# Performance work log

Hardware: AMD Instinct MI355X
Metric: run time of the kernel (lower is better)

## Reference

```python
import jax, jax.numpy as jnp
import numpy as np

B, N, VF, EF, DV, DE, LN = 64, 64, 32, 16, 128, 128, 4
EPS_INNER = 128.0  # BatchNorm1d(MAX_N, internal_d_vert): 2nd positional arg is eps (faithful to source bug)
EPS_BN = 1e-5


def gev_layer(v_in, e_in, evW, evb, eW, eb, vW, vb, relu=True):
    act = jax.nn.relu if relu else (lambda x: x)
    ev = v_in @ evW + evb                                   # [B,N,De]
    # outer_v_sum: ev.unsqueeze(1) + ev.unsqueeze(2) -> [B,N,N,De]
    e_out = act(e_in @ eW + eb + ev[:, None, :, :] + ev[:, :, None, :])
    per_v_e = e_out.sum(axis=1)                             # sum-aggregate over dim 1
    v_out = act(jnp.concatenate([per_v_e, v_in], axis=-1) @ vW + vb)
    return v_out, e_out


def bn_flat(v, g, b):
    # BatchNorm1d(N*VF) on [B, N*VF] in training mode (biased var)
    x = v.reshape(-1, N * VF)
    mu = x.mean(axis=0)
    var = x.var(axis=0)
    x = (x - mu) * jax.lax.rsqrt(var + EPS_BN) * g + b
    return x.reshape(-1, N, VF)


def bn_inner(v, g, b):
    # BatchNorm1d(MAX_N, eps=128) on [B, N, D]: channels are the N axis, stats over (B, D)
    mu = v.mean(axis=(0, 2), keepdims=True)
    var = v.var(axis=(0, 2), keepdims=True)
    return (v - mu) * jax.lax.rsqrt(var + EPS_INNER) * g[None, :, None] + b[None, :, None]


def setup_inputs() -> dict:
    key = jax.random.key(0)
    ks = jax.random.split(key, 24)
    s = 0.01  # force_lin_init with init_noise=0.01, biases zero
    nrm = lambda k, shp: jax.random.normal(k, shp, dtype=jnp.float32) * s
    inp = {
        "v": jax.random.normal(ks[0], (B, N, VF), dtype=jnp.float32),
        "e": jax.random.normal(ks[1], (B, N, N, EF), dtype=jnp.float32),
        "bn_in_g": jnp.ones((N * VF,), jnp.float32),
        "bn_in_b": jnp.zeros((N * VF,), jnp.float32),
        "g1_evW": nrm(ks[2], (VF, DE)), "g1_evb": jnp.zeros((DE,), jnp.float32),
        "g1_eW": nrm(ks[3], (EF, DE)), "g1_eb": jnp.zeros((DE,), jnp.float32),
        "g1_vW": nrm(ks[4], (VF + DE, DV)), "g1_vb": jnp.zeros((DV,), jnp.float32),
        "inn_evW": nrm(ks[5], (LN, DV, DE)), "inn_evb": jnp.zeros((LN, DE), jnp.float32),
        "inn_eW": nrm(ks[6], (LN, DE, DE)), "inn_eb": jnp.zeros((LN, DE), jnp.float32),
        "inn_vW": nrm(ks[7], (LN, DV + DE, DV)), "inn_vb": jnp.zeros((LN, DV), jnp.float32),
        "bn_g": jnp.ones((LN, N), jnp.float32),
        "bn_b": jnp.zeros((LN, N), jnp.float32),
        "g3_evW": nrm(ks[8], (DV, 1)), "g3_evb": jnp.zeros((1,), jnp.float32),
        "g3_eW": nrm(ks[9], (DE, 1)), "g3_eb": jnp.zeros((1,), jnp.float32),
        "g3_vW": nrm(ks[10], (DV + 1, 1)), "g3_vb": jnp.zeros((1,), jnp.float32),
    }
    return inp


def reference(v, e, bn_in_g, bn_in_b, g1_evW, g1_evb, g1_eW, g1_eb, g1_vW, g1_vb,
              inn_evW, inn_evb, inn_eW, inn_eb, inn_vW, inn_vb, bn_g, bn_b,
              g3_evW, g3_evb, g3_eW, g3_eb, g3_vW, g3_vb):
    v = bn_flat(v, bn_in_g, bn_in_b)
    v, e = gev_layer(v, e, g1_evW, g1_evb, g1_eW, g1_eb, g1_vW, g1_vb)
    for i in range(LN):
        v_next, e_next = gev_layer(v, e, inn_evW[i], inn_evb[i], inn_eW[i], inn_eb[i], inn_vW[i], inn_vb[i])
        v = v_next + v  # resnet
        e = e_next + e
        v = bn_inner(v, bn_g[i], bn_b[i])
    v, e = gev_layer(v, e, g3_evW, g3_evb, g3_eW, g3_eb, g3_vW, g3_vb, relu=False)
    return v, e
```

## Files before the change

kernel.cpp:

```cpp
#include <hip/hip_runtime.h>
#include <hip/hip_bf16.h>


typedef __bf16 bf16_t;
typedef __bf16 bf16x8 __attribute__((ext_vector_type(8)));
typedef __bf16 bf16x4 __attribute__((ext_vector_type(4)));
typedef float f32x4 __attribute__((ext_vector_type(4)));

__device__ __forceinline__ void bar_lgkm() {
  asm volatile("s_waitcnt lgkmcnt(0)\n\ts_barrier" ::: "memory");
}

__global__ __launch_bounds__(256) void k_prep(const float* __restrict__ vin,
    const float* __restrict__ g, const float* __restrict__ bt,
    const float* __restrict__ eW, float* __restrict__ v0,
    bf16_t* __restrict__ Wt, float* __restrict__ stats) {
  const int blk = blockIdx.x, tid = threadIdx.x;
  if (blk < 8) {
    int ch = blk * 256 + tid;
    float s = 0.f, s2 = 0.f;
    for (int b = 0; b < 64; ++b) { float x = vin[b * 2048 + ch]; s += x; s2 += x * x; }
    float mu = s * (1.f / 64.f);
    float var = s2 * (1.f / 64.f) - mu * mu;
    float sc = rsqrtf(var + 1e-5f) * g[ch];
    float bb = bt[ch];
    for (int b = 0; b < 64; ++b) {
      float x = vin[b * 2048 + ch];
      v0[b * 2048 + ch] = (x - mu) * sc + bb;
    }
  } else if (blk < 264) {
    int idx = (blk - 8) * 256 + tid;
    int l = idx >> 14, r = idx & 16383, n = r >> 7, k = r & 127;
    Wt[idx] = (bf16_t)eW[(l << 14) + (k << 7) + n];
  } else {
    for (int i = tid; i < 512; i += 256) stats[i] = 0.f;
  }
}

template <int K>
__global__ __launch_bounds__(256) void k_ev(const float* __restrict__ v_in,
    const float* __restrict__ W, const float* __restrict__ bias,
    float* __restrict__ out) {
  __shared__ float rows_s[8][K];
  const int r0 = blockIdx.x * 8;
  const int tid = threadIdx.x;
  const int c = tid & 127, h = tid >> 7;
  for (int idx = tid; idx < 8 * K; idx += 256) {
    int rr = idx / K, kk = idx % K;
    rows_s[rr][kk] = v_in[(r0 + rr) * K + kk];
  }
  __syncthreads();
  float acc[4];
  const float bv = bias[c];
#pragma unroll
  for (int r = 0; r < 4; ++r) acc[r] = bv;
  for (int k4 = 0; k4 < K; k4 += 4) {
    float w0 = W[(k4 + 0) * 128 + c], w1 = W[(k4 + 1) * 128 + c];
    float w2 = W[(k4 + 2) * 128 + c], w3 = W[(k4 + 3) * 128 + c];
#pragma unroll
    for (int r = 0; r < 4; ++r) {
      float4 x = *(const float4*)&rows_s[h * 4 + r][k4];
      acc[r] += x.x * w0 + x.y * w1 + x.z * w2 + x.w * w3;
    }
  }
#pragma unroll
  for (int r = 0; r < 4; ++r) out[(r0 + h * 4 + r) * 128 + c] = acc[r];
}

__global__ __launch_bounds__(256) void k_evbn(float* __restrict__ v,
    const float* __restrict__ stats, const float* __restrict__ g,
    const float* __restrict__ bt, const float* __restrict__ W,
    const float* __restrict__ bias, float* __restrict__ out) {
  __shared__ float rows_s[8][128];
  const int r0 = blockIdx.x * 8;
  const int tid = threadIdx.x;
  const int c = tid & 127, h = tid >> 7;
#pragma unroll
  for (int u = 0; u < 4; ++u) {
    int idx = u * 256 + tid;
    int rr = idx >> 7, k = idx & 127;
    int n = (r0 + rr) & 63;
    float mu = stats[n] * (1.f / 8192.f);
    float var = stats[64 + n] * (1.f / 8192.f) - mu * mu;
    float sc = rsqrtf(var + 128.f) * g[n];
    float x = (v[(r0 + rr) * 128 + k] - mu) * sc + bt[n];
    rows_s[rr][k] = x;
    v[(r0 + rr) * 128 + k] = x;
  }
  __syncthreads();
  float acc[4];
  const float bv = bias[c];
#pragma unroll
  for (int r = 0; r < 4; ++r) acc[r] = bv;
  for (int k4 = 0; k4 < 128; k4 += 4) {
    float w0 = W[(k4 + 0) * 128 + c], w1 = W[(k4 + 1) * 128 + c];
    float w2 = W[(k4 + 2) * 128 + c], w3 = W[(k4 + 3) * 128 + c];
#pragma unroll
    for (int r = 0; r < 4; ++r) {
      float4 x = *(const float4*)&rows_s[h * 4 + r][k4];
      acc[r] += x.x * w0 + x.y * w1 + x.z * w2 + x.w * w3;
    }
  }
#pragma unroll
  for (int r = 0; r < 4; ++r) out[(r0 + h * 4 + r) * 128 + c] = acc[r];
}

__global__ __launch_bounds__(256) void k_edge_g1(const float* __restrict__ e0,
    const float* __restrict__ eW, const float* __restrict__ eb,
    const float* __restrict__ ev, bf16_t* __restrict__ e_ws,
    float* __restrict__ pve) {
  __shared__ bf16_t A0s[2][64][40];
  __shared__ bf16_t Os[2][64][136];
  const int b = blockIdx.x >> 5, j0 = (blockIdx.x & 31) * 2;
  const int tid = threadIdx.x;
  const int lane = tid & 63, w = tid >> 6;
  const int quad = lane >> 4, l16 = lane & 15;
#pragma unroll
  for (int t = 0; t < 2; ++t) {
    int idx = tid + t * 256;
    int row = idx >> 3, off = (idx & 7) * 4;
    int jc = off >> 4, k = off & 15;
    f32x4 x = *(const f32x4*)&e0[((b * 64 + row) * 64 + j0) * 16 + off];
    bf16x4 y;
#pragma unroll
    for (int r = 0; r < 4; ++r) y[r] = (bf16_t)x[r];
    *(bf16x4*)&A0s[jc][row][k] = y;
    bf16x4 z = {(bf16_t)0.f, (bf16_t)0.f, (bf16_t)0.f, (bf16_t)0.f};
    *(bf16x4*)&A0s[jc][row][16 + k] = z;
  }
  const int c0[2] = {w * 32 + quad * 4, w * 32 + 16 + quad * 4};
  bf16x8 wf[2];
#pragma unroll
  for (int nt = 0; nt < 2; ++nt) {
    const int c = w * 32 + nt * 16 + l16;
#pragma unroll
    for (int jj = 0; jj < 8; ++jj)
      wf[nt][jj] = (quad < 2) ? (bf16_t)eW[(quad * 8 + jj) * 128 + c] : (bf16_t)0.f;
  }
  f32x4 acc[2][4][2];
  {
    f32x4 ebv[2], evj[2][2], evi[4][2];
#pragma unroll
    for (int nt = 0; nt < 2; ++nt) {
      ebv[nt] = *(const f32x4*)&eb[c0[nt]];
#pragma unroll
      for (int jc = 0; jc < 2; ++jc)
        evj[jc][nt] = *(const f32x4*)&ev[(b * 64 + j0 + jc) * 128 + c0[nt]];
#pragma unroll
      for (int mt = 0; mt < 4; ++mt)
        evi[mt][nt] = *(const f32x4*)&ev[(b * 64 + mt * 16 + l16) * 128 + c0[nt]];
    }
#pragma unroll
    for (int jc = 0; jc < 2; ++jc)
#pragma unroll
      for (int mt = 0; mt < 4; ++mt)
#pragma unroll
        for (int nt = 0; nt < 2; ++nt)
          acc[jc][mt][nt] = ebv[nt] + evj[jc][nt] + evi[mt][nt];
  }
  __syncthreads();
#pragma unroll
  for (int jc = 0; jc < 2; ++jc) {
#pragma unroll
    for (int mt = 0; mt < 4; ++mt) {
      bf16x8 ef = *(const bf16x8*)&A0s[jc][mt * 16 + l16][quad * 8];
#pragma unroll
      for (int nt = 0; nt < 2; ++nt)
        acc[jc][mt][nt] = __builtin_amdgcn_mfma_f32_16x16x32_bf16(wf[nt], ef, acc[jc][mt][nt], 0, 0, 0);
    }
  }
#pragma unroll
  for (int jc = 0; jc < 2; ++jc) {
#pragma unroll
    for (int nt = 0; nt < 2; ++nt) {
      f32x4 ps = {0.f, 0.f, 0.f, 0.f};
#pragma unroll
      for (int mt = 0; mt < 4; ++mt) {
        const int i = mt * 16 + l16;
        bf16x4 outv;
#pragma unroll
        for (int r = 0; r < 4; ++r) {
          float vv = fmaxf(acc[jc][mt][nt][r], 0.f);
          ps[r] += vv;
          outv[r] = (bf16_t)vv;
        }
        *(bf16x4*)&Os[jc][i][c0[nt]] = outv;
      }
#pragma unroll
      for (int m = 1; m <= 8; m <<= 1) {
#pragma unroll
        for (int r = 0; r < 4; ++r) ps[r] += __shfl_xor(ps[r], m);
      }
      if (l16 == 0) *(f32x4*)&pve[(b * 64 + j0 + jc) * 128 + c0[nt]] = ps;
    }
  }
  __syncthreads();
  {
    bf16_t* ebase = &e_ws[((size_t)(b * 64 + j0) * 64) * 128];
#pragma unroll
    for (int t = 0; t < 8; ++t) {
      int idx = tid + t * 256;
      *(int4*)&ebase[idx * 8] =
          *(const int4*)&Os[idx >> 10][(idx >> 4) & 63][(idx & 15) * 8];
    }
  }
}

__global__ __launch_bounds__(256) void k_vg1_ev(const float* __restrict__ pve,
    const float* __restrict__ v0, const float* __restrict__ vW,
    const float* __restrict__ vb, const float* __restrict__ evW,
    const float* __restrict__ evb, float* __restrict__ v, float* __restrict__ ev) {
  __shared__ float in_s[8][160];
  __shared__ float vr[8][128];
  const int r0 = blockIdx.x * 8;
  const int tid = threadIdx.x;
  const int c = tid & 127, h = tid >> 7;
#pragma unroll
  for (int u = 0; u < 4; ++u) {
    int idx = u * 256 + tid;
    int rr = idx >> 7, k = idx & 127;
    in_s[rr][k] = pve[(r0 + rr) * 128 + k];
  }
  {
    int rr = tid >> 5, k = tid & 31;
    in_s[rr][128 + k] = v0[(r0 + rr) * 32 + k];
  }
  __syncthreads();
  float acc[4];
  const float bv = vb[c];
#pragma unroll
  for (int r = 0; r < 4; ++r) acc[r] = bv;
  for (int k4 = 0; k4 < 160; k4 += 4) {
    float w0 = vW[(k4 + 0) * 128 + c], w1 = vW[(k4 + 1) * 128 + c];
    float w2 = vW[(k4 + 2) * 128 + c], w3 = vW[(k4 + 3) * 128 + c];
#pragma unroll
    for (int r = 0; r < 4; ++r) {
      float4 x = *(const float4*)&in_s[h * 4 + r][k4];
      acc[r] += x.x * w0 + x.y * w1 + x.z * w2 + x.w * w3;
    }
  }
#pragma unroll
  for (int r = 0; r < 4; ++r) {
    float val = fmaxf(acc[r], 0.f);
    vr[h * 4 + r][c] = val;
    v[(r0 + h * 4 + r) * 128 + c] = val;
  }
  __syncthreads();
  float acc2[4];
  const float bv2 = evb[c];
#pragma unroll
  for (int r = 0; r < 4; ++r) acc2[r] = bv2;
  for (int k4 = 0; k4 < 128; k4 += 4) {
    float w0 = evW[(k4 + 0) * 128 + c], w1 = evW[(k4 + 1) * 128 + c];
    float w2 = evW[(k4 + 2) * 128 + c], w3 = evW[(k4 + 3) * 128 + c];
#pragma unroll
    for (int r = 0; r < 4; ++r) {
      float4 x = *(const float4*)&vr[h * 4 + r][k4];
      acc2[r] += x.x * w0 + x.y * w1 + x.z * w2 + x.w * w3;
    }
  }
#pragma unroll
  for (int r = 0; r < 4; ++r) ev[(r0 + h * 4 + r) * 128 + c] = acc2[r];
}

template <bool LAST>
__global__ __launch_bounds__(256) void k_edge_inner(bf16_t* __restrict__ e_ws,
    const bf16_t* __restrict__ Wt, const float* __restrict__ eb,
    const float* __restrict__ ev, float* __restrict__ pve,
    const float* __restrict__ eW3, float* __restrict__ edt) {
  __shared__ bf16_t As[2][64][136];
  __shared__ float W3s[128];
  const int b = blockIdx.x >> 5, j0 = (blockIdx.x & 31) * 2;
  const int tid = threadIdx.x;
  const int lane = tid & 63, w = tid >> 6;
  const int quad = lane >> 4, l16 = lane & 15;
  bf16_t* ebase = &e_ws[((size_t)(b * 64 + j0) * 64) * 128];
  int4 stg[8];
#pragma unroll
  for (int t = 0; t < 8; ++t) {
    int idx = tid + t * 256;
    stg[t] = *(const int4*)&ebase[idx * 8];
  }
  if (LAST) {
    if (tid < 128) W3s[tid] = eW3[tid];
  }
  bf16x8 wf[2][4];
#pragma unroll
  for (int nt = 0; nt < 2; ++nt)
#pragma unroll
    for (int ks = 0; ks < 4; ++ks)
      wf[nt][ks] = *(const bf16x8*)&Wt[(w * 32 + nt * 16 + l16) * 128 + ks * 32 + quad * 8];
  const int c0[2] = {w * 32 + quad * 4, w * 32 + 16 + quad * 4};
  f32x4 acc[2][4][2];
  {
    f32x4 ebv[2], evj[2][2], evi[4][2];
#pragma unroll
    for (int nt = 0; nt < 2; ++nt) {
      ebv[nt] = *(const f32x4*)&eb[c0[nt]];
#pragma unroll
      for (int jc = 0; jc < 2; ++jc)
        evj[jc][nt] = *(const f32x4*)&ev[(b * 64 + j0 + jc) * 128 + c0[nt]];
#pragma unroll
      for (int mt = 0; mt < 4; ++mt)
        evi[mt][nt] = *(const f32x4*)&ev[(b * 64 + mt * 16 + l16) * 128 + c0[nt]];
    }
#pragma unroll
    for (int jc = 0; jc < 2; ++jc)
#pragma unroll
      for (int mt = 0; mt < 4; ++mt)
#pragma unroll
        for (int nt = 0; nt < 2; ++nt)
          acc[jc][mt][nt] = ebv[nt] + evj[jc][nt] + evi[mt][nt];
  }
#pragma unroll
  for (int t = 0; t < 8; ++t) {
    int idx = tid + t * 256;
    *(int4*)&As[idx >> 10][(idx >> 4) & 63][(idx & 15) * 8] = stg[t];
  }
  bar_lgkm();
#pragma unroll
  for (int ks = 0; ks < 4; ++ks) {
    bf16x8 ef[2][4];
#pragma unroll
    for (int jc = 0; jc < 2; ++jc)
#pragma unroll
      for (int mt = 0; mt < 4; ++mt)
        ef[jc][mt] = *(const bf16x8*)&As[jc][mt * 16 + l16][ks * 32 + quad * 8];
#pragma unroll
    for (int jc = 0; jc < 2; ++jc)
#pragma unroll
      for (int mt = 0; mt < 4; ++mt)
#pragma unroll
        for (int nt = 0; nt < 2; ++nt)
          acc[jc][mt][nt] = __builtin_amdgcn_mfma_f32_16x16x32_bf16(wf[nt][ks], ef[jc][mt], acc[jc][mt][nt], 0, 0, 0);
  }
  bar_lgkm();
#pragma unroll
  for (int jc = 0; jc < 2; ++jc) {
#pragma unroll
    for (int nt = 0; nt < 2; ++nt) {
      f32x4 ps = {0.f, 0.f, 0.f, 0.f};
#pragma unroll
      for (int mt = 0; mt < 4; ++mt) {
        const int i = mt * 16 + l16;
        bf16x4 eo = *(const bf16x4*)&As[jc][i][c0[nt]];
        bf16x4 outv;
#pragma unroll
        for (int r = 0; r < 4; ++r) {
          float vv = fmaxf(acc[jc][mt][nt][r], 0.f);
          ps[r] += vv;
          outv[r] = (bf16_t)(vv + (float)eo[r]);
        }
        *(bf16x4*)&As[jc][i][c0[nt]] = outv;
      }
#pragma unroll
      for (int m = 1; m <= 8; m <<= 1) {
#pragma unroll
        for (int r = 0; r < 4; ++r) ps[r] += __shfl_xor(ps[r], m);
      }
      if (l16 == 0) *(f32x4*)&pve[(b * 64 + j0 + jc) * 128 + c0[nt]] = ps;
    }
  }
  bar_lgkm();
  if (!LAST) {
#pragma unroll
    for (int t = 0; t < 8; ++t) {
      int idx = tid + t * 256;
      *(int4*)&ebase[idx * 8] =
          *(const int4*)&As[idx >> 10][(idx >> 4) & 63][(idx & 15) * 8];
    }
  } else {
    const int i = tid >> 2, q = tid & 3;
#pragma unroll
    for (int jc = 0; jc < 2; ++jc) {
      float d = 0.f;
#pragma unroll
      for (int t = 0; t < 4; ++t) {
        bf16x8 x = *(const bf16x8*)&As[jc][i][q * 32 + t * 8];
#pragma unroll
        for (int u = 0; u < 8; ++u) d += (float)x[u] * W3s[q * 32 + t * 8 + u];
      }
      d += __shfl_xor(d, 1);
      d += __shfl_xor(d, 2);
      if (q == 0) edt[(b * 64 + j0 + jc) * 64 + i] = d;
    }
  }
}

__global__ __launch_bounds__(256) void k_v_inner(const float* __restrict__ pve,
    float* __restrict__ v, const float* __restrict__ vW,
    const float* __restrict__ vb, float* __restrict__ stats) {
  __shared__ float in_s[8][256];
  __shared__ float outs[8][132];
  __shared__ float part[16][2];
  const int r0 = blockIdx.x * 8;
  const int tid = threadIdx.x;
  const int c = tid & 127, h = tid >> 7;
#pragma unroll
  for (int u = 0; u < 4; ++u) {
    int idx = u * 256 + tid;
    int rr = idx >> 7, k = idx & 127;
    in_s[rr][k] = pve[(r0 + rr) * 128 + k];
    in_s[rr][128 + k] = v[(r0 + rr) * 128 + k];
  }
  __syncthreads();
  float acc[4];
  const float bv = vb[c];
#pragma unroll
  for (int r = 0; r < 4; ++r) acc[r] = bv;
  for (int k4 = 0; k4 < 256; k4 += 4) {
    float w0 = vW[(k4 + 0) * 128 + c], w1 = vW[(k4 + 1) * 128 + c];
    float w2 = vW[(k4 + 2) * 128 + c], w3 = vW[(k4 + 3) * 128 + c];
#pragma unroll
    for (int r = 0; r < 4; ++r) {
      float4 x = *(const float4*)&in_s[h * 4 + r][k4];
      acc[r] += x.x * w0 + x.y * w1 + x.z * w2 + x.w * w3;
    }
  }
#pragma unroll
  for (int r = 0; r < 4; ++r) {
    float val = fmaxf(acc[r], 0.f) + in_s[h * 4 + r][128 + c];
    outs[h * 4 + r][c] = val;
    v[(r0 + h * 4 + r) * 128 + c] = val;
  }
  __syncthreads();
  if (tid < 16) {
    int rr = tid >> 1, half = tid & 1;
    float s = 0.f, s2 = 0.f;
    for (int k = 0; k < 64; ++k) {
      float x = outs[rr][half * 64 + k];
      s += x; s2 += x * x;
    }
    part[tid][0] = s;
    part[tid][1] = s2;
  }
  __syncthreads();
  if (tid < 8) {
    int n = (r0 + tid) & 63;
    atomicAdd(&stats[n], part[tid * 2][0] + part[tid * 2 + 1][0]);
    atomicAdd(&stats[64 + n], part[tid * 2][1] + part[tid * 2 + 1][1]);
  }
}

__global__ __launch_bounds__(256) void k_g3(const float* __restrict__ vv,
    const float* __restrict__ stats3, const float* __restrict__ g,
    const float* __restrict__ bt, const float* __restrict__ evW3,
    const float* __restrict__ evb3, const float* __restrict__ eb3,
    const float* __restrict__ edt, const float* __restrict__ vW3,
    const float* __restrict__ vb3, float* __restrict__ out_v,
    float* __restrict__ out_e) {
  __shared__ float vbn[64][132];
  __shared__ float edts[64][68];
  __shared__ float scs[64], shs[64];
  __shared__ float W3e[128];
  __shared__ float vWs[132];
  __shared__ float ev3s[64];
  __shared__ float pj[4][64];
  const int b = blockIdx.x, tid = threadIdx.x;
  if (tid < 64) {
    float mu = stats3[tid] * (1.f / 8192.f);
    float var = stats3[64 + tid] * (1.f / 8192.f) - mu * mu;
    float sc = rsqrtf(var + 128.f) * g[tid];
    scs[tid] = sc;
    shs[tid] = bt[tid] - mu * sc;
  }
  if (tid < 128) W3e[tid] = evW3[tid];
  if (tid < 129) vWs[tid] = vW3[tid];
  __syncthreads();
#pragma unroll
  for (int t = 0; t < 8; ++t) {
    int idx = t * 1024 + tid * 4;
    int row = idx >> 7, cc = idx & 127;
    f32x4 x = *(const f32x4*)&vv[(b * 64 + row) * 128 + cc];
    *(f32x4*)&vbn[row][cc] = x * scs[row] + shs[row];
  }
#pragma unroll
  for (int t = 0; t < 4; ++t) {
    int idx = t * 1024 + tid * 4;
    int j = idx >> 6, i = idx & 63;
    *(f32x4*)&edts[j][i] = *(const f32x4*)&edt[(b * 64 + j) * 64 + i];
  }
  __syncthreads();
  {
    int i = tid >> 2, q = tid & 3;
    float d = 0.f;
#pragma unroll
    for (int u = 0; u < 32; ++u) d += vbn[i][q * 32 + u] * W3e[q * 32 + u];
    d += __shfl_xor(d, 1);
    d += __shfl_xor(d, 2);
    if (q == 0) ev3s[i] = d + evb3[0];
  }
  __syncthreads();
  {
    int q = tid >> 6, j = tid & 63;
    float s = 0.f;
    const float e3 = eb3[0];
    const float evj = ev3s[j];
#pragma unroll
    for (int r = 0; r < 16; ++r) {
      int i = q * 16 + r;
      float val = edts[j][i] + e3 + ev3s[i] + evj;
      out_e[(b * 64 + i) * 64 + j] = val;
      s += val;
    }
    pj[q][j] = s;
  }
  __syncthreads();
  {
    int n = tid >> 2, q = tid & 3;
    float d = 0.f;
#pragma unroll
    for (int u = 0; u < 32; ++u) d += vbn[n][q * 32 + u] * vWs[1 + q * 32 + u];
    d += __shfl_xor(d, 1);
    d += __shfl_xor(d, 2);
    if (q == 0) {
      float p3 = pj[0][n] + pj[1][n] + pj[2][n] + pj[3][n];
      out_v[b * 64 + n] = d + p3 * vWs[0] + vb3[0];
    }
  }
}

extern "C" void kernel_launch(void* const* d_in, const int* in_sizes, int n_in,
                              void* d_out, int out_size, void* d_ws, size_t ws_size,
                              hipStream_t stream) {
  const float* in_v    = (const float*)d_in[0];
  const float* in_e    = (const float*)d_in[1];
  const float* bn_in_g = (const float*)d_in[2];
  const float* bn_in_b = (const float*)d_in[3];
  const float* g1_evW  = (const float*)d_in[4];
  const float* g1_evb  = (const float*)d_in[5];
  const float* g1_eW   = (const float*)d_in[6];
  const float* g1_eb   = (const float*)d_in[7];
  const float* g1_vW   = (const float*)d_in[8];
  const float* g1_vb   = (const float*)d_in[9];
  const float* inn_evW = (const float*)d_in[10];
  const float* inn_evb = (const float*)d_in[11];
  const float* inn_eW  = (const float*)d_in[12];
  const float* inn_eb  = (const float*)d_in[13];
  const float* inn_vW  = (const float*)d_in[14];
  const float* inn_vb  = (const float*)d_in[15];
  const float* bn_g    = (const float*)d_in[16];
  const float* bn_b    = (const float*)d_in[17];
  const float* g3_evW  = (const float*)d_in[18];
  const float* g3_evb  = (const float*)d_in[19];
  const float* g3_eW   = (const float*)d_in[20];
  const float* g3_eb   = (const float*)d_in[21];
  const float* g3_vW   = (const float*)d_in[22];
  const float* g3_vb   = (const float*)d_in[23];

  char* ws = (char*)d_ws;
  bf16_t* e_ws = (bf16_t*)(ws);
  float* v     = (float*)(ws + 67108864);
  float* ev    = (float*)(ws + 69206016);
  float* pve   = (float*)(ws + 71303168);
  float* v0    = (float*)(ws + 73400320);
  bf16_t* Wt   = (bf16_t*)(ws + 73924608);
  float* edt   = (float*)(ws + 74055680);
  float* stats = (float*)(ws + 75104256);

  float* out_v = (float*)d_out;
  float* out_e = (float*)d_out + 4096;

  k_prep<<<265, 256, 0, stream>>>(in_v, bn_in_g, bn_in_b, inn_eW, v0, Wt, stats);

  k_ev<32><<<512, 256, 0, stream>>>(v0, g1_evW, g1_evb, ev);
  k_edge_g1<<<2048, 256, 0, stream>>>(in_e, g1_eW, g1_eb, ev, e_ws, pve);
  k_vg1_ev<<<512, 256, 0, stream>>>(pve, v0, g1_vW, g1_vb, inn_evW, inn_evb, v, ev);

  for (int l = 0; l < 4; ++l) {
    if (l > 0)
      k_evbn<<<512, 256, 0, stream>>>(v, stats + (l - 1) * 128, bn_g + (l - 1) * 64,
                                      bn_b + (l - 1) * 64, inn_evW + l * 16384,
                                      inn_evb + l * 128, ev);
    if (l < 3)
      k_edge_inner<false><<<2048, 256, 0, stream>>>(e_ws, Wt + l * 16384,
          inn_eb + l * 128, ev, pve, g3_eW, edt);
    else
      k_edge_inner<true><<<2048, 256, 0, stream>>>(e_ws, Wt + l * 16384,
          inn_eb + l * 128, ev, pve, g3_eW, edt);
    k_v_inner<<<512, 256, 0, stream>>>(pve, v, inn_vW + l * 32768, inn_vb + l * 128,
                                       stats + l * 128);
  }

  k_g3<<<64, 256, 0, stream>>>(v, stats + 384, bn_g + 192, bn_b + 192,
                               g3_evW, g3_evb, g3_eb, edt, g3_vW, g3_vb,
                               out_v, out_e);
}
```

Before: 366.4 us.

## Fuse vertex update into inner edge kernel and parallelize input batchnorm

The per-layer vertex MLP (concat of summed edges and vertex features, matmul, relu, residual, BN stats) moves into the tail of the inner edge kernel. Each block already holds the per-vertex edge sums for its two j rows in shared memory. This removes four kernel launches and the pve global round trip. The cost is that each of the 2048 blocks now reads the full 256x128 vW matrix from global/L2, where the old kernel read it 512 times, and the edge kernel's tail gets longer. The input batchnorm in k_prep is also spread over 64 blocks with a shared-memory reduction instead of 8 serial blocks.

```diff
diff --git a/kernel.cpp b/kernel.cpp
--- a/kernel.cpp
+++ b/kernel.cpp
@@ -15,21 +15,40 @@
     const float* __restrict__ g, const float* __restrict__ bt,
     const float* __restrict__ eW, float* __restrict__ v0,
     bf16_t* __restrict__ Wt, float* __restrict__ stats) {
+  __shared__ float red[8][32][2];
+  __shared__ float scb[32], shb[32];
   const int blk = blockIdx.x, tid = threadIdx.x;
-  if (blk < 8) {
-    int ch = blk * 256 + tid;
+  if (blk < 64) {
+    const int chq = tid & 31, bq = tid >> 5;
+    const int ch = blk * 32 + chq;
     float s = 0.f, s2 = 0.f;
-    for (int b = 0; b < 64; ++b) { float x = vin[b * 2048 + ch]; s += x; s2 += x * x; }
-    float mu = s * (1.f / 64.f);
-    float var = s2 * (1.f / 64.f) - mu * mu;
-    float sc = rsqrtf(var + 1e-5f) * g[ch];
-    float bb = bt[ch];
-    for (int b = 0; b < 64; ++b) {
-      float x = vin[b * 2048 + ch];
-      v0[b * 2048 + ch] = (x - mu) * sc + bb;
-    }
-  } else if (blk < 264) {
-    int idx = (blk - 8) * 256 + tid;
+#pragma unroll
+    for (int t = 0; t < 8; ++t) {
+      float x = vin[(bq * 8 + t) * 2048 + ch];
+      s += x; s2 += x * x;
+    }
+    red[bq][chq][0] = s;
+    red[bq][chq][1] = s2;
+    __syncthreads();
+    if (tid < 32) {
+      float S = 0.f, S2 = 0.f;
+#pragma unroll
+      for (int q = 0; q < 8; ++q) { S += red[q][tid][0]; S2 += red[q][tid][1]; }
+      float mu = S * (1.f / 64.f);
+      float var = S2 * (1.f / 64.f) - mu * mu;
+      float sc = rsqrtf(var + 1e-5f) * g[blk * 32 + tid];
+      scb[tid] = sc;
+      shb[tid] = bt[blk * 32 + tid] - mu * sc;
+    }
+    __syncthreads();
+    const float sc = scb[chq], sh = shb[chq];
+#pragma unroll
+    for (int t = 0; t < 8; ++t) {
+      int b = bq * 8 + t;
+      v0[b * 2048 + ch] = vin[b * 2048 + ch] * sc + sh;
+    }
+  } else if (blk < 320) {
+    int idx = (blk - 64) * 256 + tid;
     int l = idx >> 14, r = idx & 16383, n = r >> 7, k = r & 127;
     Wt[idx] = (bf16_t)eW[(l << 14) + (k << 7) + n];
   } else {
@@ -266,10 +285,14 @@
 template <bool LAST>
 __global__ __launch_bounds__(256) void k_edge_inner(bf16_t* __restrict__ e_ws,
     const bf16_t* __restrict__ Wt, const float* __restrict__ eb,
-    const float* __restrict__ ev, float* __restrict__ pve,
-    const float* __restrict__ eW3, float* __restrict__ edt) {
+    const float* __restrict__ ev, float* __restrict__ vglob,
+    const float* __restrict__ vW, const float* __restrict__ vb,
+    float* __restrict__ stats, const float* __restrict__ eW3,
+    float* __restrict__ edt) {
   __shared__ bf16_t As[2][64][136];
   __shared__ float W3s[128];
+  __shared__ float pves[2][128];
+  __shared__ float vrow[2][128];
   const int b = blockIdx.x >> 5, j0 = (blockIdx.x & 31) * 2;
   const int tid = threadIdx.x;
   const int lane = tid & 63, w = tid >> 6;
@@ -281,6 +304,7 @@
     int idx = tid + t * 256;
     stg[t] = *(const int4*)&ebase[idx * 8];
   }
+  vrow[tid >> 7][tid & 127] = vglob[(b * 64 + j0 + (tid >> 7)) * 128 + (tid & 127)];
   if (LAST) {
     if (tid < 128) W3s[tid] = eW3[tid];
   }
@@ -358,7 +382,7 @@
 #pragma unroll
         for (int r = 0; r < 4; ++r) ps[r] += __shfl_xor(ps[r], m);
       }
-      if (l16 == 0) *(f32x4*)&pve[(b * 64 + j0 + jc) * 128 + c0[nt]] = ps;
+      if (l16 == 0) *(f32x4*)&pves[jc][c0[nt]] = ps;
     }
   }
   bar_lgkm();
@@ -385,60 +409,53 @@
       if (q == 0) edt[(b * 64 + j0 + jc) * 64 + i] = d;
     }
   }
-}
-
-__global__ __launch_bounds__(256) void k_v_inner(const float* __restrict__ pve,
-    float* __restrict__ v, const float* __restrict__ vW,
-    const float* __restrict__ vb, float* __restrict__ stats) {
-  __shared__ float in_s[8][256];
-  __shared__ float outs[8][132];
-  __shared__ float part[16][2];
-  const int r0 = blockIdx.x * 8;
-  const int tid = threadIdx.x;
-  const int c = tid & 127, h = tid >> 7;
-#pragma unroll
-  for (int u = 0; u < 4; ++u) {
-    int idx = u * 256 + tid;
-    int rr = idx >> 7, k = idx & 127;
-    in_s[rr][k] = pve[(r0 + rr) * 128 + k];
-    in_s[rr][128 + k] = v[(r0 + rr) * 128 + k];
-  }
-  __syncthreads();
-  float acc[4];
-  const float bv = vb[c];
-#pragma unroll
-  for (int r = 0; r < 4; ++r) acc[r] = bv;
-  for (int k4 = 0; k4 < 256; k4 += 4) {
-    float w0 = vW[(k4 + 0) * 128 + c], w1 = vW[(k4 + 1) * 128 + c];
-    float w2 = vW[(k4 + 2) * 128 + c], w3 = vW[(k4 + 3) * 128 + c];
-#pragma unroll
-    for (int r = 0; r < 4; ++r) {
-      float4 x = *(const float4*)&in_s[h * 4 + r][k4];
-      acc[r] += x.x * w0 + x.y * w1 + x.z * w2 + x.w * w3;
-    }
-  }
-#pragma unroll
-  for (int r = 0; r < 4; ++r) {
-    float val = fmaxf(acc[r], 0.f) + in_s[h * 4 + r][128 + c];
-    outs[h * 4 + r][c] = val;
-    v[(r0 + h * 4 + r) * 128 + c] = val;
-  }
-  __syncthreads();
-  if (tid < 16) {
-    int rr = tid >> 1, half = tid & 1;
-    float s = 0.f, s2 = 0.f;
-    for (int k = 0; k < 64; ++k) {
-      float x = outs[rr][half * 64 + k];
-      s += x; s2 += x * x;
-    }
-    part[tid][0] = s;
-    part[tid][1] = s2;
-  }
-  __syncthreads();
-  if (tid < 8) {
-    int n = (r0 + tid) & 63;
-    atomicAdd(&stats[n], part[tid * 2][0] + part[tid * 2 + 1][0]);
-    atomicAdd(&stats[64 + n], part[tid * 2][1] + part[tid * 2 + 1][1]);
+  {
+    const int jc = tid >> 7, c = tid & 127;
+    float a = vb[c];
+    for (int k0 = 0; k0 < 128; k0 += 16) {
+      float wv[16];
+#pragma unroll
+      for (int t = 0; t < 16; ++t) wv[t] = vW[(k0 + t) * 128 + c];
+      f32x4 p0 = *(const f32x4*)&pves[jc][k0];
+      f32x4 p1 = *(const f32x4*)&pves[jc][k0 + 4];
+      f32x4 p2 = *(const f32x4*)&pves[jc][k0 + 8];
+      f32x4 p3 = *(const f32x4*)&pves[jc][k0 + 12];
+#pragma unroll
+      for (int u = 0; u < 4; ++u) {
+        a += p0[u] * wv[u];
+        a += p1[u] * wv[4 + u];
+        a += p2[u] * wv[8 + u];
+        a += p3[u] * wv[12 + u];
+      }
+    }
+    for (int k0 = 0; k0 < 128; k0 += 16) {
+      float wv[16];
+#pragma unroll
+      for (int t = 0; t < 16; ++t) wv[t] = vW[(128 + k0 + t) * 128 + c];
+      f32x4 p0 = *(const f32x4*)&vrow[jc][k0];
+      f32x4 p1 = *(const f32x4*)&vrow[jc][k0 + 4];
+      f32x4 p2 = *(const f32x4*)&vrow[jc][k0 + 8];
+      f32x4 p3 = *(const f32x4*)&vrow[jc][k0 + 12];
+#pragma unroll
+      for (int u = 0; u < 4; ++u) {
+        a += p0[u] * wv[u];
+        a += p1[u] * wv[4 + u];
+        a += p2[u] * wv[8 + u];
+        a += p3[u] * wv[12 + u];
+      }
+    }
+    float val = fmaxf(a, 0.f) + vrow[jc][c];
+    vglob[(b * 64 + j0 + jc) * 128 + c] = val;
+    float s = val, s2 = val * val;
+#pragma unroll
+    for (int m = 1; m < 64; m <<= 1) {
+      s += __shfl_xor(s, m);
+      s2 += __shfl_xor(s2, m);
+    }
+    if (lane == 0) {
+      atomicAdd(&stats[j0 + jc], s);
+      atomicAdd(&stats[64 + j0 + jc], s2);
+    }
   }
 }
 
@@ -561,7 +578,7 @@
   float* out_v = (float*)d_out;
   float* out_e = (float*)d_out + 4096;
 
-  k_prep<<<265, 256, 0, stream>>>(in_v, bn_in_g, bn_in_b, inn_eW, v0, Wt, stats);
+  k_prep<<<321, 256, 0, stream>>>(in_v, bn_in_g, bn_in_b, inn_eW, v0, Wt, stats);
 
   k_ev<32><<<512, 256, 0, stream>>>(v0, g1_evW, g1_evb, ev);
   k_edge_g1<<<2048, 256, 0, stream>>>(in_e, g1_eW, g1_eb, ev, e_ws, pve);
@@ -574,12 +591,12 @@
                                       inn_evb + l * 128, ev);
     if (l < 3)
       k_edge_inner<false><<<2048, 256, 0, stream>>>(e_ws, Wt + l * 16384,
-          inn_eb + l * 128, ev, pve, g3_eW, edt);
+          inn_eb + l * 128, ev, v, inn_vW + l * 32768, inn_vb + l * 128,
+          stats + l * 128, g3_eW, edt);
     else
       k_edge_inner<true><<<2048, 256, 0, stream>>>(e_ws, Wt + l * 16384,
-          inn_eb + l * 128, ev, pve, g3_eW, edt);
-    k_v_inner<<<512, 256, 0, stream>>>(pve, v, inn_vW + l * 32768, inn_vb + l * 128,
-                                       stats + l * 128);
+          inn_eb + l * 128, ev, v, inn_vW + l * 32768, inn_vb + l * 128,
+          stats + l * 128, g3_eW, edt);
   }
 
   k_g3<<<64, 256, 0, stream>>>(v, stats + 384, bn_g + 192, bn_b + 192,
```

After: 517.6 us. +41.2%, slower.

## Halve edge-inner tile to one j per block and parallelize input batchnorm

Applied to the files above, without the earlier changes.

The inner edge kernel now has each block process a single j row (64x128 bf16 tile) instead of two, doubling the grid to 4096 blocks. LDS use and register pressure drop, which should allow more resident blocks per CU and better latency hiding. The cost is that each block reloads the weight fragments and ev rows for half as much work. Separately, the input batchnorm prep is spread over 64 blocks with an LDS reduction across batch slices instead of 8 blocks that each loop serially over 64 batches.

```diff
diff --git a/kernel.cpp b/kernel.cpp
--- a/kernel.cpp
+++ b/kernel.cpp
@@ -15,21 +15,40 @@
     const float* __restrict__ g, const float* __restrict__ bt,
     const float* __restrict__ eW, float* __restrict__ v0,
     bf16_t* __restrict__ Wt, float* __restrict__ stats) {
+  __shared__ float red[8][32][2];
+  __shared__ float scb[32], shb[32];
   const int blk = blockIdx.x, tid = threadIdx.x;
-  if (blk < 8) {
-    int ch = blk * 256 + tid;
+  if (blk < 64) {
+    const int chq = tid & 31, bq = tid >> 5;
+    const int ch = blk * 32 + chq;
     float s = 0.f, s2 = 0.f;
-    for (int b = 0; b < 64; ++b) { float x = vin[b * 2048 + ch]; s += x; s2 += x * x; }
-    float mu = s * (1.f / 64.f);
-    float var = s2 * (1.f / 64.f) - mu * mu;
-    float sc = rsqrtf(var + 1e-5f) * g[ch];
-    float bb = bt[ch];
-    for (int b = 0; b < 64; ++b) {
-      float x = vin[b * 2048 + ch];
-      v0[b * 2048 + ch] = (x - mu) * sc + bb;
-    }
-  } else if (blk < 264) {
-    int idx = (blk - 8) * 256 + tid;
+#pragma unroll
+    for (int t = 0; t < 8; ++t) {
+      float x = vin[(bq * 8 + t) * 2048 + ch];
+      s += x; s2 += x * x;
+    }
+    red[bq][chq][0] = s;
+    red[bq][chq][1] = s2;
+    __syncthreads();
+    if (tid < 32) {
+      float S = 0.f, S2 = 0.f;
+#pragma unroll
+      for (int q = 0; q < 8; ++q) { S += red[q][tid][0]; S2 += red[q][tid][1]; }
+      float mu = S * (1.f / 64.f);
+      float var = S2 * (1.f / 64.f) - mu * mu;
+      float sc = rsqrtf(var + 1e-5f) * g[blk * 32 + tid];
+      scb[tid] = sc;
+      shb[tid] = bt[blk * 32 + tid] - mu * sc;
+    }
+    __syncthreads();
+    const float sc = scb[chq], sh = shb[chq];
+#pragma unroll
+    for (int t = 0; t < 8; ++t) {
+      int b = bq * 8 + t;
+      v0[b * 2048 + ch] = vin[b * 2048 + ch] * sc + sh;
+    }
+  } else if (blk < 320) {
+    int idx = (blk - 64) * 256 + tid;
     int l = idx >> 14, r = idx & 16383, n = r >> 7, k = r & 127;
     Wt[idx] = (bf16_t)eW[(l << 14) + (k << 7) + n];
   } else {
@@ -268,16 +287,16 @@
     const bf16_t* __restrict__ Wt, const float* __restrict__ eb,
     const float* __restrict__ ev, float* __restrict__ pve,
     const float* __restrict__ eW3, float* __restrict__ edt) {
-  __shared__ bf16_t As[2][64][136];
+  __shared__ bf16_t As[64][136];
   __shared__ float W3s[128];
-  const int b = blockIdx.x >> 5, j0 = (blockIdx.x & 31) * 2;
+  const int b = blockIdx.x >> 6, j = blockIdx.x & 63;
   const int tid = threadIdx.x;
   const int lane = tid & 63, w = tid >> 6;
   const int quad = lane >> 4, l16 = lane & 15;
-  bf16_t* ebase = &e_ws[((size_t)(b * 64 + j0) * 64) * 128];
-  int4 stg[8];
-#pragma unroll
-  for (int t = 0; t < 8; ++t) {
+  bf16_t* ebase = &e_ws[((size_t)(b * 64 + j) * 64) * 128];
+  int4 stg[4];
+#pragma unroll
+  for (int t = 0; t < 4; ++t) {
     int idx = tid + t * 256;
     stg[t] = *(const int4*)&ebase[idx * 8];
   }
@@ -291,99 +310,84 @@
     for (int ks = 0; ks < 4; ++ks)
       wf[nt][ks] = *(const bf16x8*)&Wt[(w * 32 + nt * 16 + l16) * 128 + ks * 32 + quad * 8];
   const int c0[2] = {w * 32 + quad * 4, w * 32 + 16 + quad * 4};
-  f32x4 acc[2][4][2];
-  {
-    f32x4 ebv[2], evj[2][2], evi[4][2];
+  f32x4 acc[4][2];
+  {
+    f32x4 ebv[2], evj[2], evi[4][2];
 #pragma unroll
     for (int nt = 0; nt < 2; ++nt) {
       ebv[nt] = *(const f32x4*)&eb[c0[nt]];
-#pragma unroll
-      for (int jc = 0; jc < 2; ++jc)
-        evj[jc][nt] = *(const f32x4*)&ev[(b * 64 + j0 + jc) * 128 + c0[nt]];
+      evj[nt] = *(const f32x4*)&ev[(b * 64 + j) * 128 + c0[nt]];
 #pragma unroll
       for (int mt = 0; mt < 4; ++mt)
         evi[mt][nt] = *(const f32x4*)&ev[(b * 64 + mt * 16 + l16) * 128 + c0[nt]];
     }
 #pragma unroll
-    for (int jc = 0; jc < 2; ++jc)
-#pragma unroll
-      for (int mt = 0; mt < 4; ++mt)
-#pragma unroll
-        for (int nt = 0; nt < 2; ++nt)
-          acc[jc][mt][nt] = ebv[nt] + evj[jc][nt] + evi[mt][nt];
-  }
-#pragma unroll
-  for (int t = 0; t < 8; ++t) {
+    for (int mt = 0; mt < 4; ++mt)
+#pragma unroll
+      for (int nt = 0; nt < 2; ++nt)
+        acc[mt][nt] = ebv[nt] + evj[nt] + evi[mt][nt];
+  }
+#pragma unroll
+  for (int t = 0; t < 4; ++t) {
     int idx = tid + t * 256;
-    *(int4*)&As[idx >> 10][(idx >> 4) & 63][(idx & 15) * 8] = stg[t];
+    *(int4*)&As[idx >> 4][(idx & 15) * 8] = stg[t];
   }
   bar_lgkm();
 #pragma unroll
   for (int ks = 0; ks < 4; ++ks) {
-    bf16x8 ef[2][4];
-#pragma unroll
-    for (int jc = 0; jc < 2; ++jc)
-#pragma unroll
-      for (int mt = 0; mt < 4; ++mt)
-        ef[jc][mt] = *(const bf16x8*)&As[jc][mt * 16 + l16][ks * 32 + quad * 8];
-#pragma unroll
-    for (int jc = 0; jc < 2; ++jc)
-#pragma unroll
-      for (int mt = 0; mt < 4; ++mt)
-#pragma unroll
-        for (int nt = 0; nt < 2; ++nt)
-          acc[jc][mt][nt] = __builtin_amdgcn_mfma_f32_16x16x32_bf16(wf[nt][ks], ef[jc][mt], acc[jc][mt][nt], 0, 0, 0);
+    bf16x8 ef[4];
+#pragma unroll
+    for (int mt = 0; mt < 4; ++mt)
+      ef[mt] = *(const bf16x8*)&As[mt * 16 + l16][ks * 32 + quad * 8];
+#pragma unroll
+    for (int mt = 0; mt < 4; ++mt)
+#pragma unroll
+      for (int nt = 0; nt < 2; ++nt)
+        acc[mt][nt] = __builtin_amdgcn_mfma_f32_16x16x32_bf16(wf[nt][ks], ef[mt], acc[mt][nt], 0, 0, 0);
   }
   bar_lgkm();
 #pragma unroll
-  for (int jc = 0; jc < 2; ++jc) {
-#pragma unroll
-    for (int nt = 0; nt < 2; ++nt) {
-      f32x4 ps = {0.f, 0.f, 0.f, 0.f};
-#pragma unroll
-      for (int mt = 0; mt < 4; ++mt) {
-        const int i = mt * 16 + l16;
-        bf16x4 eo = *(const bf16x4*)&As[jc][i][c0[nt]];
-        bf16x4 outv;
-#pragma unroll
-        for (int r = 0; r < 4; ++r) {
-          float vv = fmaxf(acc[jc][mt][nt][r], 0.f);
-          ps[r] += vv;
-          outv[r] = (bf16_t)(vv + (float)eo[r]);
-        }
-        *(bf16x4*)&As[jc][i][c0[nt]] = outv;
+  for (int nt = 0; nt < 2; ++nt) {
+    f32x4 ps = {0.f, 0.f, 0.f, 0.f};
+#pragma unroll
+    for (int mt = 0; mt < 4; ++mt) {
+      const int i = mt * 16 + l16;
+      bf16x4 eo = *(const bf16x4*)&As[i][c0[nt]];
+      bf16x4 outv;
+#pragma unroll
+      for (int r = 0; r < 4; ++r) {
+        float vv = fmaxf(acc[mt][nt][r], 0.f);
+        ps[r] += vv;
+        outv[r] = (bf16_t)(vv + (float)eo[r]);
       }
-#pragma unroll
-      for (int m = 1; m <= 8; m <<= 1) {
-#pragma unroll
-        for (int r = 0; r < 4; ++r) ps[r] += __shfl_xor(ps[r], m);
-      }
-      if (l16 == 0) *(f32x4*)&pve[(b * 64 + j0 + jc) * 128 + c0[nt]] = ps;
-    }
+      *(bf16x4*)&As[i][c0[nt]] = outv;
+    }
+#pragma unroll
+    for (int m = 1; m <= 8; m <<= 1) {
+#pragma unroll
+      for (int r = 0; r < 4; ++r) ps[r] += __shfl_xor(ps[r], m);
+    }
+    if (l16 == 0) *(f32x4*)&pve[(b * 64 + j) * 128 + c0[nt]] = ps;
   }
   bar_lgkm();
   if (!LAST) {
 #pragma unroll
-    for (int t = 0; t < 8; ++t) {
+    for (int t = 0; t < 4; ++t) {
       int idx = tid + t * 256;
-      *(int4*)&ebase[idx * 8] =
-          *(const int4*)&As[idx >> 10][(idx >> 4) & 63][(idx & 15) * 8];
+      *(int4*)&ebase[idx * 8] = *(const int4*)&As[idx >> 4][(idx & 15) * 8];
     }
   } else {
     const int i = tid >> 2, q = tid & 3;
-#pragma unroll
-    for (int jc = 0; jc < 2; ++jc) {
-      float d = 0.f;
-#pragma unroll
-      for (int t = 0; t < 4; ++t) {
-        bf16x8 x = *(const bf16x8*)&As[jc][i][q * 32 + t * 8];
-#pragma unroll
-        for (int u = 0; u < 8; ++u) d += (float)x[u] * W3s[q * 32 + t * 8 + u];
-      }
-      d += __shfl_xor(d, 1);
-      d += __shfl_xor(d, 2);
-      if (q == 0) edt[(b * 64 + j0 + jc) * 64 + i] = d;
-    }
+    float d = 0.f;
+#pragma unroll
+    for (int t = 0; t < 4; ++t) {
+      bf16x8 x = *(const bf16x8*)&As[i][q * 32 + t * 8];
+#pragma unroll
+      for (int u = 0; u < 8; ++u) d += (float)x[u] * W3s[q * 32 + t * 8 + u];
+    }
+    d += __shfl_xor(d, 1);
+    d += __shfl_xor(d, 2);
+    if (q == 0) edt[(b * 64 + j) * 64 + i] = d;
   }
 }
 
@@ -561,7 +565,7 @@
   float* out_v = (float*)d_out;
   float* out_e = (float*)d_out + 4096;
 
-  k_prep<<<265, 256, 0, stream>>>(in_v, bn_in_g, bn_in_b, inn_eW, v0, Wt, stats);
+  k_prep<<<321, 256, 0, stream>>>(in_v, bn_in_g, bn_in_b, inn_eW, v0, Wt, stats);
 
   k_ev<32><<<512, 256, 0, stream>>>(v0, g1_evW, g1_evb, ev);
   k_edge_g1<<<2048, 256, 0, stream>>>(in_e, g1_eW, g1_eb, ev, e_ws, pve);
@@ -573,10 +577,10 @@
                                       bn_b + (l - 1) * 64, inn_evW + l * 16384,
                                       inn_evb + l * 128, ev);
     if (l < 3)
-      k_edge_inner<false><<<2048, 256, 0, stream>>>(e_ws, Wt + l * 16384,
+      k_edge_inner<false><<<4096, 256, 0, stream>>>(e_ws, Wt + l * 16384,
           inn_eb + l * 128, ev, pve, g3_eW, edt);
     else
-      k_edge_inner<true><<<2048, 256, 0, stream>>>(e_ws, Wt + l * 16384,
+      k_edge_inner<true><<<4096, 256, 0, stream>>>(e_ws, Wt + l * 16384,
           inn_eb + l * 128, ev, pve, g3_eW, edt);
     k_v_inner<<<512, 256, 0, stream>>>(pve, v, inn_vW + l * 32768, inn_vb + l * 128,
                                        stats + l * 128);
```

Result: slower. 399.7 us (+9.1%).
